# Optimization experiments

Hardware: AMD Instinct MI355X
Metric: run time of the kernel (lower is better)

The kernel has to match this reference:

```python
import jax, jax.numpy as jnp
import numpy as np

NA = 100000   # node_num_a
NB = 100000   # node_num_b
D = 128       # a_dim == b_dim
E = 1_600_000 # edges, avg degree 16


def setup_inputs() -> dict:
    key = jax.random.key(0)
    k1, k2, k3, k4, k5, k6 = jax.random.split(key, 6)
    feature_a = jax.random.normal(k1, (NA, D), dtype=jnp.float32)
    feature_b = jax.random.normal(k2, (NB, D), dtype=jnp.float32)
    src = jax.random.randint(k3, (E, 1), 0, NA)
    dst = jax.random.randint(k4, (E, 1), 0, NB)
    edges = jnp.concatenate([src, dst], axis=1).astype(jnp.int64)
    W_mlp = jax.random.normal(k5, (D, D), dtype=jnp.float32) / np.sqrt(D)
    b_mlp = jnp.zeros((D,), dtype=jnp.float32)
    a_vec = jax.random.normal(k6, (2 * D, 1), dtype=jnp.float32) / np.sqrt(2 * D)
    return {"feature_a": feature_a, "feature_b": feature_b, "edges": edges,
            "W_mlp": W_mlp, "b_mlp": b_mlp, "a_vec": a_vec}


def reference(feature_a, feature_b, edges, W_mlp, b_mlp, a_vec):
    """AttentionAggregator.forward: edge-gathered attention + segment aggregation."""
    na, a_dim = feature_a.shape
    # nn.Linear: x @ W.T + b
    new_emb = feature_b @ W_mlp.T + b_mlp                      # [Nb, D]
    # einsum(cat([fa[src], new_emb[dst]]), a) == fa[src]@a_top + new_emb[dst]@a_bot
    a_top = a_vec[:a_dim, 0]
    a_bot = a_vec[a_dim:, 0]
    s_a = feature_a @ a_top                                    # [Na]
    s_b = new_emb @ a_bot                                      # [Nb]
    src = edges[:, 0]
    dst = edges[:, 1]
    score = s_a[src] + s_b[dst]                                # [E]
    # F.elu(x, alpha=0.1) then exp
    ALPHA = 0.1
    elu = jnp.where(score > 0, score, ALPHA * jnp.expm1(score))
    w = jnp.exp(elu)                                           # [E]
    # sparse.mm(matrix, ones)  -> per-row sum of edge weights (duplicates coalesce by sum)
    row_sum = jax.ops.segment_sum(w, src, num_segments=na)     # [Na]
    row_sum = jnp.where(row_sum == 0, 1.0, row_sum)
    # sparse.mm(matrix, new_emb) -> weighted neighbor aggregation
    msg = w[:, None] * new_emb[dst]                            # [E, D]
    agg = jax.ops.segment_sum(msg, src, num_segments=na)       # [Na, D]
    return agg / row_sum[:, None]
```

## Files before the change

kernel.cpp:

```cpp
#include <hip/hip_runtime.h>
#include <math.h>

#define NA 100000
#define NB 100000
#define DIM 128
#define NEDGE 1600000
#define ALPHA 0.1f
#define BCAP 32
#define OVF_CAP 65536

#define WS_NEBF   0
#define WS_WBF    25600000
#define WS_SA     25632768
#define WS_SB     26032768
#define WS_CNT    26432768
#define WS_FLAG   26832768
#define WS_OVF    26832832
#define WS_PAIRS  27357120

using bf16x8 = __attribute__((ext_vector_type(8))) short;
using f32x16 = __attribute__((ext_vector_type(16))) float;

__device__ inline short f2bf(float f) {
    union { float f; unsigned u; } v; v.f = f;
    const unsigned r = (v.u + 0x7FFFu + ((v.u >> 16) & 1u)) >> 16;
    return (short)r;
}

__global__ void k_prep(const int* __restrict__ edges32, int* __restrict__ flags,
                       const float* __restrict__ W, short* __restrict__ wbf) {
    if (blockIdx.x == 0) {
        __shared__ int any;
        if (threadIdx.x == 0) any = 0;
        __syncthreads();
        if (edges32[2 * threadIdx.x + 1] != 0) atomicOr(&any, 1);
        __syncthreads();
        if (threadIdx.x == 0) flags[0] = (any == 0) ? 1 : 0;
    } else {
        const int i = (blockIdx.x - 1) * 256 + threadIdx.x;
        if (i < DIM * DIM) wbf[i] = f2bf(W[i]);
    }
}

__global__ __launch_bounds__(256) void k_newemb(
    const float* __restrict__ fb, const short* __restrict__ wbf,
    const float* __restrict__ bias, const float* __restrict__ avec,
    short* __restrict__ nebf, float* __restrict__ s_b)
{
    const int wv = threadIdx.x >> 6;
    const int lane = threadIdx.x & 63;
    const int tile = blockIdx.x * 4 + wv;
    const int row0 = tile * 32;
    if (row0 >= NB) return;
    const int l31 = lane & 31;
    const int h = lane >> 5;

    f32x16 acc[4];
    #pragma unroll
    for (int nt = 0; nt < 4; ++nt)
        #pragma unroll
        for (int r = 0; r < 16; ++r) acc[nt][r] = 0.f;

    const float* arow = fb + (size_t)(row0 + l31) * DIM;

    #pragma unroll 2
    for (int s = 0; s < 8; ++s) {
        const int k0 = s * 16 + h * 8;
        const float4 a0 = *(const float4*)(arow + k0);
        const float4 a1 = *(const float4*)(arow + k0 + 4);
        bf16x8 af;
        af[0] = f2bf(a0.x); af[1] = f2bf(a0.y); af[2] = f2bf(a0.z); af[3] = f2bf(a0.w);
        af[4] = f2bf(a1.x); af[5] = f2bf(a1.y); af[6] = f2bf(a1.z); af[7] = f2bf(a1.w);
        #pragma unroll
        for (int nt = 0; nt < 4; ++nt) {
            const int n = nt * 32 + l31;
            const bf16x8 bf = *(const bf16x8*)(wbf + n * DIM + k0);
            acc[nt] = __builtin_amdgcn_mfma_f32_32x32x16_bf16(af, bf, acc[nt], 0, 0, 0);
        }
    }

    float ab[4], bs[4];
    #pragma unroll
    for (int nt = 0; nt < 4; ++nt) {
        ab[nt] = avec[DIM + nt * 32 + l31];
        bs[nt] = bias[nt * 32 + l31];
    }
    float sb[16];
    #pragma unroll
    for (int r = 0; r < 16; ++r) {
        const int row = row0 + (r & 3) + 8 * (r >> 2) + 4 * h;
        float p = 0.f;
        #pragma unroll
        for (int nt = 0; nt < 4; ++nt) {
            const float v = acc[nt][r] + bs[nt];
            nebf[(size_t)row * DIM + nt * 32 + l31] = f2bf(v);
            p += v * ab[nt];
        }
        #pragma unroll
        for (int m = 16; m; m >>= 1) p += __shfl_xor(p, m, 64);
        sb[r] = p;
    }
    if (l31 == 0) {
        #pragma unroll
        for (int r = 0; r < 16; ++r)
            s_b[row0 + (r & 3) + 8 * (r >> 2) + 4 * h] = sb[r];
    }
}

__global__ __launch_bounds__(256) void k_sa(
    const float* __restrict__ fa, const float* __restrict__ avec,
    float* __restrict__ s_a)
{
    const int row = blockIdx.x * 4 + (threadIdx.x >> 6);
    if (row >= NA) return;
    const int lane = threadIdx.x & 63;
    const float2 v = *(const float2*)(fa + (size_t)row * DIM + 2 * lane);
    const float2 a = *(const float2*)(avec + 2 * lane);
    float p = v.x * a.x + v.y * a.y;
    #pragma unroll
    for (int m = 32; m; m >>= 1) p += __shfl_xor(p, m, 64);
    if (lane == 0) s_a[row] = p;
}

__global__ __launch_bounds__(256) void k_scatter(
    const void* __restrict__ edges, const int* __restrict__ flags,
    int* __restrict__ cnt, int* __restrict__ bucket,
    int2* __restrict__ ovf, int* __restrict__ ovfcnt)
{
    const int e = blockIdx.x * 256 + threadIdx.x;
    if (e >= NEDGE) return;
    int src, dst;
    if (flags[0]) {
        const int4 v = ((const int4*)edges)[e];
        src = v.x; dst = v.z;
    } else {
        const int2 v = ((const int2*)edges)[e];
        src = v.x; dst = v.y;
    }
    const int pos = atomicAdd(&cnt[src], 1);
    if (pos < BCAP) {
        bucket[(src << 5) + pos] = dst;
    } else {
        const int o = atomicAdd(ovfcnt, 1);
        if (o < OVF_CAP) ovf[o] = make_int2(src, dst);
    }
}

#define ACC8(u, wt)                                                             \
    a0 += (wt) * __uint_as_float((u).x << 16);                                  \
    a1 += (wt) * __uint_as_float((u).x & 0xFFFF0000u);                          \
    a2 += (wt) * __uint_as_float((u).y << 16);                                  \
    a3 += (wt) * __uint_as_float((u).y & 0xFFFF0000u);                          \
    a4 += (wt) * __uint_as_float((u).z << 16);                                  \
    a5 += (wt) * __uint_as_float((u).z & 0xFFFF0000u);                          \
    a6 += (wt) * __uint_as_float((u).w << 16);                                  \
    a7 += (wt) * __uint_as_float((u).w & 0xFFFF0000u);

__device__ inline float edge_w(float sar, float sb) {
    const float sc = sar + sb;
    const float el = (sc > 0.f) ? sc : ALPHA * expm1f(sc);
    return expf(el);
}

__global__ __launch_bounds__(256) void k_rowagg(
    const int* __restrict__ cnt, const int* __restrict__ bucket_all,
    const float* __restrict__ s_a, const float* __restrict__ s_b,
    const unsigned* __restrict__ nebf, const int2* __restrict__ ovf,
    const int* __restrict__ flags, float* __restrict__ out)
{
    const int row = blockIdx.x * 4 + (threadIdx.x >> 6);
    if (row >= NA) return;
    const int lane = threadIdx.x & 63;
    const int l = lane & 15;
    const int q = lane >> 4;
    const int c = cnt[row];
    const int cb = (c > BCAP) ? BCAP : c;
    const int* bucket = bucket_all + (row << 5);
    const float sar = s_a[row];

    float a0 = 0.f, a1 = 0.f, a2 = 0.f, a3 = 0.f;
    float a4 = 0.f, a5 = 0.f, a6 = 0.f, a7 = 0.f, wsum = 0.f;
    int i = q;
    for (; i + 4 < cb; i += 8) {
        const int d0 = bucket[i];
        const int d1 = bucket[i + 4];
        const uint4 u0 = *(const uint4*)(nebf + (size_t)d0 * (DIM / 2) + 4 * l);
        const uint4 u1 = *(const uint4*)(nebf + (size_t)d1 * (DIM / 2) + 4 * l);
        const float w0 = edge_w(sar, s_b[d0]);
        const float w1 = edge_w(sar, s_b[d1]);
        ACC8(u0, w0)
        ACC8(u1, w1)
        wsum += w0 + w1;
    }
    for (; i < cb; i += 4) {
        const int d = bucket[i];
        const uint4 u = *(const uint4*)(nebf + (size_t)d * (DIM / 2) + 4 * l);
        const float wv = edge_w(sar, s_b[d]);
        ACC8(u, wv)
        wsum += wv;
    }
    int novf = flags[1];
    novf = (novf > OVF_CAP) ? OVF_CAP : novf;
    for (int j = q; j < novf; j += 4) {
        const int2 pe = ovf[j];
        if (pe.x == row) {
            const uint4 u = *(const uint4*)(nebf + (size_t)pe.y * (DIM / 2) + 4 * l);
            const float wv = edge_w(sar, s_b[pe.y]);
            ACC8(u, wv)
            wsum += wv;
        }
    }
    a0 += __shfl_xor(a0, 16, 64); a0 += __shfl_xor(a0, 32, 64);
    a1 += __shfl_xor(a1, 16, 64); a1 += __shfl_xor(a1, 32, 64);
    a2 += __shfl_xor(a2, 16, 64); a2 += __shfl_xor(a2, 32, 64);
    a3 += __shfl_xor(a3, 16, 64); a3 += __shfl_xor(a3, 32, 64);
    a4 += __shfl_xor(a4, 16, 64); a4 += __shfl_xor(a4, 32, 64);
    a5 += __shfl_xor(a5, 16, 64); a5 += __shfl_xor(a5, 32, 64);
    a6 += __shfl_xor(a6, 16, 64); a6 += __shfl_xor(a6, 32, 64);
    a7 += __shfl_xor(a7, 16, 64); a7 += __shfl_xor(a7, 32, 64);
    wsum += __shfl_xor(wsum, 16, 64); wsum += __shfl_xor(wsum, 32, 64);
    if (q == 0) {
        const float inv = 1.f / ((wsum == 0.f) ? 1.f : wsum);
        float* o = out + (size_t)row * DIM + 8 * l;
        *(float4*)o       = make_float4(a0 * inv, a1 * inv, a2 * inv, a3 * inv);
        *(float4*)(o + 4) = make_float4(a4 * inv, a5 * inv, a6 * inv, a7 * inv);
    }
}

extern "C" void kernel_launch(void* const* d_in, const int* in_sizes, int n_in,
                              void* d_out, int out_size, void* d_ws, size_t ws_size,
                              hipStream_t stream) {
    const float* fa    = (const float*)d_in[0];
    const float* fb    = (const float*)d_in[1];
    const void*  edges = d_in[2];
    const float* W     = (const float*)d_in[3];
    const float* bias  = (const float*)d_in[4];
    const float* avec  = (const float*)d_in[5];
    float* out = (float*)d_out;
    char* ws = (char*)d_ws;
    short* nebf  = (short*)(ws + WS_NEBF);
    short* wbf   = (short*)(ws + WS_WBF);
    float* s_a   = (float*)(ws + WS_SA);
    float* s_b   = (float*)(ws + WS_SB);
    int*   cnt   = (int*)(ws + WS_CNT);
    int*   flags = (int*)(ws + WS_FLAG);
    int2*  ovf   = (int2*)(ws + WS_OVF);
    int*   bucket= (int*)(ws + WS_PAIRS);

    (void)hipMemsetAsync(ws + WS_CNT, 0, (size_t)NA * sizeof(int) + 64, stream);
    k_prep<<<1 + (DIM * DIM + 255) / 256, 256, 0, stream>>>((const int*)edges, flags, W, wbf);
    k_newemb<<<(NB / 32 + 3) / 4, 256, 0, stream>>>(fb, wbf, bias, avec, nebf, s_b);
    k_sa<<<(NA + 3) / 4, 256, 0, stream>>>(fa, avec, s_a);
    k_scatter<<<(NEDGE + 255) / 256, 256, 0, stream>>>(edges, flags, cnt, bucket, ovf, &flags[1]);
    k_rowagg<<<(NA + 3) / 4, 256, 0, stream>>>(cnt, bucket, s_a, s_b,
                                               (const unsigned*)nebf, ovf, flags, out);
}
```

Measured before the change: 361.2 us.

## Fuse new-emb GEMM, edge scatter and s_a kernels into one launch; unroll rowagg by four

Merges three independent kernels (the new_emb MFMA GEMM, the edge bucket scatter and the s_a dot products) into a single launch that dispatches on block index ranges. The independent work can then overlap on the GPU and two launch gaps go away. It also adds a 4-way unrolled gather loop in the row aggregation so more neighbor loads are in flight at once. The costs are a fused kernel whose register budget is set by the heaviest branch (the MFMA path), which may limit occupancy for the light scatter and s_a blocks, and higher register pressure in rowagg.

Result: slower. 371.0 us (+2.7%).

```diff
diff --git a/kernel.cpp b/kernel.cpp
--- a/kernel.cpp
+++ b/kernel.cpp
@@ -17,6 +17,10 @@
 #define WS_FLAG   26832768
 #define WS_OVF    26832832
 #define WS_PAIRS  27357120
+
+#define NEWEMB_BLOCKS 782
+#define SCAT_BLOCKS   6250
+#define SA_BLOCKS     25000
 
 using bf16x8 = __attribute__((ext_vector_type(8))) short;
 using f32x16 = __attribute__((ext_vector_type(16))) float;
@@ -42,107 +46,101 @@
     }
 }
 
-__global__ __launch_bounds__(256) void k_newemb(
+__global__ __launch_bounds__(256) void k_fused(
     const float* __restrict__ fb, const short* __restrict__ wbf,
     const float* __restrict__ bias, const float* __restrict__ avec,
-    short* __restrict__ nebf, float* __restrict__ s_b)
-{
-    const int wv = threadIdx.x >> 6;
-    const int lane = threadIdx.x & 63;
-    const int tile = blockIdx.x * 4 + wv;
-    const int row0 = tile * 32;
-    if (row0 >= NB) return;
-    const int l31 = lane & 31;
-    const int h = lane >> 5;
-
-    f32x16 acc[4];
-    #pragma unroll
-    for (int nt = 0; nt < 4; ++nt)
-        #pragma unroll
-        for (int r = 0; r < 16; ++r) acc[nt][r] = 0.f;
-
-    const float* arow = fb + (size_t)(row0 + l31) * DIM;
-
-    #pragma unroll 2
-    for (int s = 0; s < 8; ++s) {
-        const int k0 = s * 16 + h * 8;
-        const float4 a0 = *(const float4*)(arow + k0);
-        const float4 a1 = *(const float4*)(arow + k0 + 4);
-        bf16x8 af;
-        af[0] = f2bf(a0.x); af[1] = f2bf(a0.y); af[2] = f2bf(a0.z); af[3] = f2bf(a0.w);
-        af[4] = f2bf(a1.x); af[5] = f2bf(a1.y); af[6] = f2bf(a1.z); af[7] = f2bf(a1.w);
-        #pragma unroll
-        for (int nt = 0; nt < 4; ++nt) {
-            const int n = nt * 32 + l31;
-            const bf16x8 bf = *(const bf16x8*)(wbf + n * DIM + k0);
-            acc[nt] = __builtin_amdgcn_mfma_f32_32x32x16_bf16(af, bf, acc[nt], 0, 0, 0);
-        }
-    }
-
-    float ab[4], bs[4];
-    #pragma unroll
-    for (int nt = 0; nt < 4; ++nt) {
-        ab[nt] = avec[DIM + nt * 32 + l31];
-        bs[nt] = bias[nt * 32 + l31];
-    }
-    float sb[16];
-    #pragma unroll
-    for (int r = 0; r < 16; ++r) {
-        const int row = row0 + (r & 3) + 8 * (r >> 2) + 4 * h;
-        float p = 0.f;
-        #pragma unroll
-        for (int nt = 0; nt < 4; ++nt) {
-            const float v = acc[nt][r] + bs[nt];
-            nebf[(size_t)row * DIM + nt * 32 + l31] = f2bf(v);
-            p += v * ab[nt];
-        }
-        #pragma unroll
-        for (int m = 16; m; m >>= 1) p += __shfl_xor(p, m, 64);
-        sb[r] = p;
-    }
-    if (l31 == 0) {
-        #pragma unroll
-        for (int r = 0; r < 16; ++r)
-            s_b[row0 + (r & 3) + 8 * (r >> 2) + 4 * h] = sb[r];
-    }
-}
-
-__global__ __launch_bounds__(256) void k_sa(
-    const float* __restrict__ fa, const float* __restrict__ avec,
-    float* __restrict__ s_a)
-{
-    const int row = blockIdx.x * 4 + (threadIdx.x >> 6);
-    if (row >= NA) return;
-    const int lane = threadIdx.x & 63;
-    const float2 v = *(const float2*)(fa + (size_t)row * DIM + 2 * lane);
-    const float2 a = *(const float2*)(avec + 2 * lane);
-    float p = v.x * a.x + v.y * a.y;
-    #pragma unroll
-    for (int m = 32; m; m >>= 1) p += __shfl_xor(p, m, 64);
-    if (lane == 0) s_a[row] = p;
-}
-
-__global__ __launch_bounds__(256) void k_scatter(
+    short* __restrict__ nebf, float* __restrict__ s_b,
     const void* __restrict__ edges, const int* __restrict__ flags,
     int* __restrict__ cnt, int* __restrict__ bucket,
-    int2* __restrict__ ovf, int* __restrict__ ovfcnt)
+    int2* __restrict__ ovf, int* __restrict__ ovfcnt,
+    const float* __restrict__ fa, float* __restrict__ s_a)
 {
-    const int e = blockIdx.x * 256 + threadIdx.x;
-    if (e >= NEDGE) return;
-    int src, dst;
-    if (flags[0]) {
-        const int4 v = ((const int4*)edges)[e];
-        src = v.x; dst = v.z;
+    const int lane = threadIdx.x & 63;
+    if (blockIdx.x < NEWEMB_BLOCKS) {
+        const int wv = threadIdx.x >> 6;
+        const int tile = blockIdx.x * 4 + wv;
+        const int row0 = tile * 32;
+        if (row0 >= NB) return;
+        const int l31 = lane & 31;
+        const int h = lane >> 5;
+
+        f32x16 acc[4];
+        #pragma unroll
+        for (int nt = 0; nt < 4; ++nt)
+            #pragma unroll
+            for (int r = 0; r < 16; ++r) acc[nt][r] = 0.f;
+
+        const float* arow = fb + (size_t)(row0 + l31) * DIM;
+
+        #pragma unroll 2
+        for (int s = 0; s < 8; ++s) {
+            const int k0 = s * 16 + h * 8;
+            const float4 a0 = *(const float4*)(arow + k0);
+            const float4 a1 = *(const float4*)(arow + k0 + 4);
+            bf16x8 af;
+            af[0] = f2bf(a0.x); af[1] = f2bf(a0.y); af[2] = f2bf(a0.z); af[3] = f2bf(a0.w);
+            af[4] = f2bf(a1.x); af[5] = f2bf(a1.y); af[6] = f2bf(a1.z); af[7] = f2bf(a1.w);
+            #pragma unroll
+            for (int nt = 0; nt < 4; ++nt) {
+                const int n = nt * 32 + l31;
+                const bf16x8 bf = *(const bf16x8*)(wbf + n * DIM + k0);
+                acc[nt] = __builtin_amdgcn_mfma_f32_32x32x16_bf16(af, bf, acc[nt], 0, 0, 0);
+            }
+        }
+
+        float ab[4], bs[4];
+        #pragma unroll
+        for (int nt = 0; nt < 4; ++nt) {
+            ab[nt] = avec[DIM + nt * 32 + l31];
+            bs[nt] = bias[nt * 32 + l31];
+        }
+        float sb[16];
+        #pragma unroll
+        for (int r = 0; r < 16; ++r) {
+            const int row = row0 + (r & 3) + 8 * (r >> 2) + 4 * h;
+            float p = 0.f;
+            #pragma unroll
+            for (int nt = 0; nt < 4; ++nt) {
+                const float v = acc[nt][r] + bs[nt];
+                nebf[(size_t)row * DIM + nt * 32 + l31] = f2bf(v);
+                p += v * ab[nt];
+            }
+            #pragma unroll
+            for (int m = 16; m; m >>= 1) p += __shfl_xor(p, m, 64);
+            sb[r] = p;
+        }
+        if (l31 == 0) {
+            #pragma unroll
+            for (int r = 0; r < 16; ++r)
+                s_b[row0 + (r & 3) + 8 * (r >> 2) + 4 * h] = sb[r];
+        }
+    } else if (blockIdx.x < NEWEMB_BLOCKS + SCAT_BLOCKS) {
+        const int e = (blockIdx.x - NEWEMB_BLOCKS) * 256 + threadIdx.x;
+        if (e >= NEDGE) return;
+        int src, dst;
+        if (flags[0]) {
+            const int4 v = ((const int4*)edges)[e];
+            src = v.x; dst = v.z;
+        } else {
+            const int2 v = ((const int2*)edges)[e];
+            src = v.x; dst = v.y;
+        }
+        const int pos = atomicAdd(&cnt[src], 1);
+        if (pos < BCAP) {
+            bucket[(src << 5) + pos] = dst;
+        } else {
+            const int o = atomicAdd(ovfcnt, 1);
+            if (o < OVF_CAP) ovf[o] = make_int2(src, dst);
+        }
     } else {
-        const int2 v = ((const int2*)edges)[e];
-        src = v.x; dst = v.y;
-    }
-    const int pos = atomicAdd(&cnt[src], 1);
-    if (pos < BCAP) {
-        bucket[(src << 5) + pos] = dst;
-    } else {
-        const int o = atomicAdd(ovfcnt, 1);
-        if (o < OVF_CAP) ovf[o] = make_int2(src, dst);
+        const int row = (blockIdx.x - NEWEMB_BLOCKS - SCAT_BLOCKS) * 4 + (threadIdx.x >> 6);
+        if (row >= NA) return;
+        const float2 v = *(const float2*)(fa + (size_t)row * DIM + 2 * lane);
+        const float2 a = *(const float2*)(avec + 2 * lane);
+        float p = v.x * a.x + v.y * a.y;
+        #pragma unroll
+        for (int m = 32; m; m >>= 1) p += __shfl_xor(p, m, 64);
+        if (lane == 0) s_a[row] = p;
     }
 }
 
@@ -181,6 +179,25 @@
     float a0 = 0.f, a1 = 0.f, a2 = 0.f, a3 = 0.f;
     float a4 = 0.f, a5 = 0.f, a6 = 0.f, a7 = 0.f, wsum = 0.f;
     int i = q;
+    for (; i + 12 < cb; i += 16) {
+        const int d0 = bucket[i];
+        const int d1 = bucket[i + 4];
+        const int d2 = bucket[i + 8];
+        const int d3 = bucket[i + 12];
+        const uint4 u0 = *(const uint4*)(nebf + (size_t)d0 * (DIM / 2) + 4 * l);
+        const uint4 u1 = *(const uint4*)(nebf + (size_t)d1 * (DIM / 2) + 4 * l);
+        const uint4 u2 = *(const uint4*)(nebf + (size_t)d2 * (DIM / 2) + 4 * l);
+        const uint4 u3 = *(const uint4*)(nebf + (size_t)d3 * (DIM / 2) + 4 * l);
+        const float w0 = edge_w(sar, s_b[d0]);
+        const float w1 = edge_w(sar, s_b[d1]);
+        const float w2 = edge_w(sar, s_b[d2]);
+        const float w3 = edge_w(sar, s_b[d3]);
+        ACC8(u0, w0)
+        ACC8(u1, w1)
+        ACC8(u2, w2)
+        ACC8(u3, w3)
+        wsum += (w0 + w1) + (w2 + w3);
+    }
     for (; i + 4 < cb; i += 8) {
         const int d0 = bucket[i];
         const int d1 = bucket[i + 4];
@@ -249,9 +266,10 @@
 
     (void)hipMemsetAsync(ws + WS_CNT, 0, (size_t)NA * sizeof(int) + 64, stream);
     k_prep<<<1 + (DIM * DIM + 255) / 256, 256, 0, stream>>>((const int*)edges, flags, W, wbf);
-    k_newemb<<<(NB / 32 + 3) / 4, 256, 0, stream>>>(fb, wbf, bias, avec, nebf, s_b);
-    k_sa<<<(NA + 3) / 4, 256, 0, stream>>>(fa, avec, s_a);
-    k_scatter<<<(NEDGE + 255) / 256, 256, 0, stream>>>(edges, flags, cnt, bucket, ovf, &flags[1]);
+    k_fused<<<NEWEMB_BLOCKS + SCAT_BLOCKS + SA_BLOCKS, 256, 0, stream>>>(
+        fb, wbf, bias, avec, nebf, s_b,
+        edges, flags, cnt, bucket, ovf, &flags[1],
+        fa, s_a);
     k_rowagg<<<(NA + 3) / 4, 256, 0, stream>>>(cnt, bucket, s_a, s_b,
                                                (const unsigned*)nebf, ovf, flags, out);
 }
```

## Compute edge weights during scatter and store them with destination in buckets

Applied to the files above, without the earlier changes.

When the workspace is large enough, the scatter kernel now computes each edge's attention weight and stores it packed with the destination index as an int2 in the row bucket. The row aggregation kernel then reads the weight directly instead of gathering s_b and evaluating expm1/exp per edge. Both aggregation kernels also get a 4-way unrolled inner loop to keep more gathers in flight. The cost is twice the bucket memory traffic and random s_a/s_b reads moved into the scatter pass. The path choice depends on the workspace size the harness provides.

Measured after the change: 360.4 us. About the same (-0.2%).

```diff
diff --git a/kernel.cpp b/kernel.cpp
--- a/kernel.cpp
+++ b/kernel.cpp
@@ -17,6 +17,8 @@
 #define WS_FLAG   26832768
 #define WS_OVF    26832832
 #define WS_PAIRS  27357120
+#define WS_TOTAL_A (27357120 + (size_t)NA * BCAP * 8)
+#define WS_TOTAL_B (27357120 + (size_t)NA * BCAP * 4)
 
 using bf16x8 = __attribute__((ext_vector_type(8))) short;
 using f32x16 = __attribute__((ext_vector_type(16))) float;
@@ -122,6 +124,38 @@
     if (lane == 0) s_a[row] = p;
 }
 
+__device__ inline float edge_w(float sar, float sb) {
+    const float sc = sar + sb;
+    const float el = (sc > 0.f) ? sc : ALPHA * expm1f(sc);
+    return expf(el);
+}
+
+__global__ __launch_bounds__(256) void k_scatter_w(
+    const void* __restrict__ edges, const int* __restrict__ flags,
+    const float* __restrict__ s_a, const float* __restrict__ s_b,
+    int* __restrict__ cnt, int2* __restrict__ bucket,
+    int2* __restrict__ ovf, int* __restrict__ ovfcnt)
+{
+    const int e = blockIdx.x * 256 + threadIdx.x;
+    if (e >= NEDGE) return;
+    int src, dst;
+    if (flags[0]) {
+        const int4 v = ((const int4*)edges)[e];
+        src = v.x; dst = v.z;
+    } else {
+        const int2 v = ((const int2*)edges)[e];
+        src = v.x; dst = v.y;
+    }
+    const float w = edge_w(s_a[src], s_b[dst]);
+    const int pos = atomicAdd(&cnt[src], 1);
+    if (pos < BCAP) {
+        bucket[(src << 5) + pos] = make_int2(dst, __float_as_int(w));
+    } else {
+        const int o = atomicAdd(ovfcnt, 1);
+        if (o < OVF_CAP) ovf[o] = make_int2(src, dst);
+    }
+}
+
 __global__ __launch_bounds__(256) void k_scatter(
     const void* __restrict__ edges, const int* __restrict__ flags,
     int* __restrict__ cnt, int* __restrict__ bucket,
@@ -156,10 +190,87 @@
     a6 += (wt) * __uint_as_float((u).w << 16);                                  \
     a7 += (wt) * __uint_as_float((u).w & 0xFFFF0000u);
 
-__device__ inline float edge_w(float sar, float sb) {
-    const float sc = sar + sb;
-    const float el = (sc > 0.f) ? sc : ALPHA * expm1f(sc);
-    return expf(el);
+#define ROWAGG_REDUCE_STORE                                                     \
+    a0 += __shfl_xor(a0, 16, 64); a0 += __shfl_xor(a0, 32, 64);                 \
+    a1 += __shfl_xor(a1, 16, 64); a1 += __shfl_xor(a1, 32, 64);                 \
+    a2 += __shfl_xor(a2, 16, 64); a2 += __shfl_xor(a2, 32, 64);                 \
+    a3 += __shfl_xor(a3, 16, 64); a3 += __shfl_xor(a3, 32, 64);                 \
+    a4 += __shfl_xor(a4, 16, 64); a4 += __shfl_xor(a4, 32, 64);                 \
+    a5 += __shfl_xor(a5, 16, 64); a5 += __shfl_xor(a5, 32, 64);                 \
+    a6 += __shfl_xor(a6, 16, 64); a6 += __shfl_xor(a6, 32, 64);                 \
+    a7 += __shfl_xor(a7, 16, 64); a7 += __shfl_xor(a7, 32, 64);                 \
+    wsum += __shfl_xor(wsum, 16, 64); wsum += __shfl_xor(wsum, 32, 64);         \
+    if (q == 0) {                                                               \
+        const float inv = 1.f / ((wsum == 0.f) ? 1.f : wsum);                   \
+        float* o = out + (size_t)row * DIM + 8 * l;                             \
+        *(float4*)o       = make_float4(a0 * inv, a1 * inv, a2 * inv, a3 * inv);\
+        *(float4*)(o + 4) = make_float4(a4 * inv, a5 * inv, a6 * inv, a7 * inv);\
+    }
+
+__global__ __launch_bounds__(256) void k_rowagg_w(
+    const int* __restrict__ cnt, const int2* __restrict__ bucket_all,
+    const float* __restrict__ s_a, const float* __restrict__ s_b,
+    const unsigned* __restrict__ nebf, const int2* __restrict__ ovf,
+    const int* __restrict__ flags, float* __restrict__ out)
+{
+    const int row = blockIdx.x * 4 + (threadIdx.x >> 6);
+    if (row >= NA) return;
+    const int lane = threadIdx.x & 63;
+    const int l = lane & 15;
+    const int q = lane >> 4;
+    const int c = cnt[row];
+    const int cb = (c > BCAP) ? BCAP : c;
+    const int2* bucket = bucket_all + (row << 5);
+
+    float a0 = 0.f, a1 = 0.f, a2 = 0.f, a3 = 0.f;
+    float a4 = 0.f, a5 = 0.f, a6 = 0.f, a7 = 0.f, wsum = 0.f;
+    int i = q;
+    for (; i + 12 < cb; i += 16) {
+        const int2 p0 = bucket[i];
+        const int2 p1 = bucket[i + 4];
+        const int2 p2 = bucket[i + 8];
+        const int2 p3 = bucket[i + 12];
+        const uint4 u0 = *(const uint4*)(nebf + (size_t)p0.x * (DIM / 2) + 4 * l);
+        const uint4 u1 = *(const uint4*)(nebf + (size_t)p1.x * (DIM / 2) + 4 * l);
+        const uint4 u2 = *(const uint4*)(nebf + (size_t)p2.x * (DIM / 2) + 4 * l);
+        const uint4 u3 = *(const uint4*)(nebf + (size_t)p3.x * (DIM / 2) + 4 * l);
+        const float w0 = __int_as_float(p0.y);
+        const float w1 = __int_as_float(p1.y);
+        const float w2 = __int_as_float(p2.y);
+        const float w3 = __int_as_float(p3.y);
+        ACC8(u0, w0) ACC8(u1, w1) ACC8(u2, w2) ACC8(u3, w3)
+        wsum += (w0 + w1) + (w2 + w3);
+    }
+    for (; i + 4 < cb; i += 8) {
+        const int2 p0 = bucket[i];
+        const int2 p1 = bucket[i + 4];
+        const uint4 u0 = *(const uint4*)(nebf + (size_t)p0.x * (DIM / 2) + 4 * l);
+        const uint4 u1 = *(const uint4*)(nebf + (size_t)p1.x * (DIM / 2) + 4 * l);
+        const float w0 = __int_as_float(p0.y);
+        const float w1 = __int_as_float(p1.y);
+        ACC8(u0, w0) ACC8(u1, w1)
+        wsum += w0 + w1;
+    }
+    for (; i < cb; i += 4) {
+        const int2 p = bucket[i];
+        const uint4 u = *(const uint4*)(nebf + (size_t)p.x * (DIM / 2) + 4 * l);
+        const float wv = __int_as_float(p.y);
+        ACC8(u, wv)
+        wsum += wv;
+    }
+    int novf = flags[1];
+    novf = (novf > OVF_CAP) ? OVF_CAP : novf;
+    const float sar = s_a[row];
+    for (int j = q; j < novf; j += 4) {
+        const int2 pe = ovf[j];
+        if (pe.x == row) {
+            const uint4 u = *(const uint4*)(nebf + (size_t)pe.y * (DIM / 2) + 4 * l);
+            const float wv = edge_w(sar, s_b[pe.y]);
+            ACC8(u, wv)
+            wsum += wv;
+        }
+    }
+    ROWAGG_REDUCE_STORE
 }
 
 __global__ __launch_bounds__(256) void k_rowagg(
@@ -181,6 +292,22 @@
     float a0 = 0.f, a1 = 0.f, a2 = 0.f, a3 = 0.f;
     float a4 = 0.f, a5 = 0.f, a6 = 0.f, a7 = 0.f, wsum = 0.f;
     int i = q;
+    for (; i + 12 < cb; i += 16) {
+        const int d0 = bucket[i];
+        const int d1 = bucket[i + 4];
+        const int d2 = bucket[i + 8];
+        const int d3 = bucket[i + 12];
+        const uint4 u0 = *(const uint4*)(nebf + (size_t)d0 * (DIM / 2) + 4 * l);
+        const uint4 u1 = *(const uint4*)(nebf + (size_t)d1 * (DIM / 2) + 4 * l);
+        const uint4 u2 = *(const uint4*)(nebf + (size_t)d2 * (DIM / 2) + 4 * l);
+        const uint4 u3 = *(const uint4*)(nebf + (size_t)d3 * (DIM / 2) + 4 * l);
+        const float w0 = edge_w(sar, s_b[d0]);
+        const float w1 = edge_w(sar, s_b[d1]);
+        const float w2 = edge_w(sar, s_b[d2]);
+        const float w3 = edge_w(sar, s_b[d3]);
+        ACC8(u0, w0) ACC8(u1, w1) ACC8(u2, w2) ACC8(u3, w3)
+        wsum += (w0 + w1) + (w2 + w3);
+    }
     for (; i + 4 < cb; i += 8) {
         const int d0 = bucket[i];
         const int d1 = bucket[i + 4];
@@ -188,8 +315,7 @@
         const uint4 u1 = *(const uint4*)(nebf + (size_t)d1 * (DIM / 2) + 4 * l);
         const float w0 = edge_w(sar, s_b[d0]);
         const float w1 = edge_w(sar, s_b[d1]);
-        ACC8(u0, w0)
-        ACC8(u1, w1)
+        ACC8(u0, w0) ACC8(u1, w1)
         wsum += w0 + w1;
     }
     for (; i < cb; i += 4) {
@@ -210,21 +336,7 @@
             wsum += wv;
         }
     }
-    a0 += __shfl_xor(a0, 16, 64); a0 += __shfl_xor(a0, 32, 64);
-    a1 += __shfl_xor(a1, 16, 64); a1 += __shfl_xor(a1, 32, 64);
-    a2 += __shfl_xor(a2, 16, 64); a2 += __shfl_xor(a2, 32, 64);
-    a3 += __shfl_xor(a3, 16, 64); a3 += __shfl_xor(a3, 32, 64);
-    a4 += __shfl_xor(a4, 16, 64); a4 += __shfl_xor(a4, 32, 64);
-    a5 += __shfl_xor(a5, 16, 64); a5 += __shfl_xor(a5, 32, 64);
-    a6 += __shfl_xor(a6, 16, 64); a6 += __shfl_xor(a6, 32, 64);
-    a7 += __shfl_xor(a7, 16, 64); a7 += __shfl_xor(a7, 32, 64);
-    wsum += __shfl_xor(wsum, 16, 64); wsum += __shfl_xor(wsum, 32, 64);
-    if (q == 0) {
-        const float inv = 1.f / ((wsum == 0.f) ? 1.f : wsum);
-        float* o = out + (size_t)row * DIM + 8 * l;
-        *(float4*)o       = make_float4(a0 * inv, a1 * inv, a2 * inv, a3 * inv);
-        *(float4*)(o + 4) = make_float4(a4 * inv, a5 * inv, a6 * inv, a7 * inv);
-    }
+    ROWAGG_REDUCE_STORE
 }
 
 extern "C" void kernel_launch(void* const* d_in, const int* in_sizes, int n_in,
@@ -245,13 +357,24 @@
     int*   cnt   = (int*)(ws + WS_CNT);
     int*   flags = (int*)(ws + WS_FLAG);
     int2*  ovf   = (int2*)(ws + WS_OVF);
-    int*   bucket= (int*)(ws + WS_PAIRS);
+
+    const bool wide = (ws_size >= WS_TOTAL_A);
 
     (void)hipMemsetAsync(ws + WS_CNT, 0, (size_t)NA * sizeof(int) + 64, stream);
     k_prep<<<1 + (DIM * DIM + 255) / 256, 256, 0, stream>>>((const int*)edges, flags, W, wbf);
     k_newemb<<<(NB / 32 + 3) / 4, 256, 0, stream>>>(fb, wbf, bias, avec, nebf, s_b);
     k_sa<<<(NA + 3) / 4, 256, 0, stream>>>(fa, avec, s_a);
-    k_scatter<<<(NEDGE + 255) / 256, 256, 0, stream>>>(edges, flags, cnt, bucket, ovf, &flags[1]);
-    k_rowagg<<<(NA + 3) / 4, 256, 0, stream>>>(cnt, bucket, s_a, s_b,
-                                               (const unsigned*)nebf, ovf, flags, out);
-}
+    if (wide) {
+        int2* bucket2 = (int2*)(ws + WS_PAIRS);
+        k_scatter_w<<<(NEDGE + 255) / 256, 256, 0, stream>>>(
+            edges, flags, s_a, s_b, cnt, bucket2, ovf, &flags[1]);
+        k_rowagg_w<<<(NA + 3) / 4, 256, 0, stream>>>(
+            cnt, bucket2, s_a, s_b, (const unsigned*)nebf, ovf, flags, out);
+    } else {
+        int* bucket = (int*)(ws + WS_PAIRS);
+        k_scatter<<<(NEDGE + 255) / 256, 256, 0, stream>>>(
+            edges, flags, cnt, bucket, ovf, &flags[1]);
+        k_rowagg<<<(NA + 3) / 4, 256, 0, stream>>>(
+            cnt, bucket, s_a, s_b, (const unsigned*)nebf, ovf, flags, out);
+    }
+}
```
